# Kernel tuning notes

Measured on AMD Instinct MI355X. Metric: run time of the kernel, lower is better.

The kernel has to match this reference:

```python
import jax, jax.numpy as jnp
import numpy as np

EPS = 1e-8


def cos_loss(a, b):
    # a, b: [n, c, h, w]; cosine distance over channel dim, mean over rest
    a_norm = jnp.sqrt((a * a).sum(1, keepdims=True))
    b_norm = jnp.sqrt((b * b).sum(1, keepdims=True))
    cossim = ((a / (a_norm + EPS)) * (b / (b_norm + EPS))).sum(1)
    return (1.0 - cossim).mean()


def nn_feat_replace(a, b):
    # a: [1, c, h, w], b: [1, c, h2, w2]
    n, c, h, w = a.shape
    a_flat = a.reshape(n, c, -1)                    # [1, c, hw]
    b_flat = b.reshape(n, c, -1)                    # [1, c, h2w2]
    # normalize along channel dim (matches argmin_cos_distance's two-eps scheme)
    b_n = b_flat / (jnp.sqrt((b_flat * b_flat).sum(1, keepdims=True) + EPS) + EPS)
    a_n = a_flat / (jnp.sqrt((a_flat * a_flat).sum(1, keepdims=True) + EPS) + EPS)
    # full cosine-distance matrix: [1, hw, h2w2]
    d_mat = 1.0 - jnp.einsum('bci,bcj->bij', a_n, b_n)
    z_best = jnp.argmin(d_mat, axis=2)              # [1, hw]
    feat = jnp.take(b_flat, z_best[0], axis=2)      # gather: [1, c, hw]
    return feat.reshape(n, c, h, w)


def setup_inputs() -> dict:
    key = jax.random.key(0)
    k1, k2 = jax.random.split(key)
    a = jax.random.normal(k1, (1, 768, 128, 128), dtype=jnp.float32)
    b = jax.random.normal(k2, (1, 768, 128, 128), dtype=jnp.float32)
    return {"a": a, "b": b}


def reference(a, b):
    target = nn_feat_replace(a, b)
    return cos_loss(a, target)
```

## Files before the change

### kernel.cpp

```cpp
#include <hip/hip_runtime.h>
#include <stdint.h>

#define HW 16384
#define CDIM 768
#define EPSF 1e-8f

typedef float f32x4  __attribute__((ext_vector_type(4)));
typedef float f32x16 __attribute__((ext_vector_type(16)));
typedef int   i32x8  __attribute__((ext_vector_type(8)));
typedef uint32_t u32x4 __attribute__((ext_vector_type(4)));

__device__ inline void async16(const void* g, void* l) {
    __builtin_amdgcn_global_load_lds(
        (const __attribute__((address_space(1))) uint32_t*)g,
        (__attribute__((address_space(3))) uint32_t*)l, 16, 0, 0);
}

__device__ inline uint32_t pk4_fp8(float v0, float v1, float v2, float v3) {
    uint32_t r = __builtin_amdgcn_cvt_pk_fp8_f32(v0, v1, 0, false);
    r = __builtin_amdgcn_cvt_pk_fp8_f32(v2, v3, r, true);
    return r;
}

__global__ void __launch_bounds__(256)
transpose_fp8_norm(const float* __restrict__ a, const float* __restrict__ b,
                   uint8_t* __restrict__ at8, uint8_t* __restrict__ bn8,
                   float* __restrict__ sumsq_a, float* __restrict__ sumsq_b) {
    const int z = blockIdx.z;
    const float* src = z ? b : a;
    uint8_t* dst = z ? bn8 : at8;
    float* sums = z ? sumsq_b : sumsq_a;
    const float mult = z ? 8.0f : 16.0f;

    __shared__ float tile[64][65];
    const int s0 = blockIdx.x * 64, c0 = blockIdx.y * 64;
    const int tx = threadIdx.x & 63, ty = threadIdx.x >> 6;
#pragma unroll
    for (int p = 0; p < 16; ++p) {
        int cl = p * 4 + ty;
        tile[cl][tx] = src[(size_t)(c0 + cl) * HW + s0 + tx];
    }
    __syncthreads();

    const int chgrp = tx & 15, rowsub = tx >> 4;
    uint32_t* dst32 = (uint32_t*)dst;
#pragma unroll
    for (int p = 0; p < 4; ++p) {
        int sl = p * 16 + ty * 4 + rowsub;
        float v0 = tile[chgrp * 4 + 0][sl];
        float v1 = tile[chgrp * 4 + 1][sl];
        float v2 = tile[chgrp * 4 + 2][sl];
        float v3 = tile[chgrp * 4 + 3][sl];
        float part = v0 * v0 + v1 * v1 + v2 * v2 + v3 * v3;
        dst32[(size_t)(s0 + sl) * (CDIM / 4) + (c0 >> 2) + chgrp] =
            pk4_fp8(v0 * mult, v1 * mult, v2 * mult, v3 * mult);
#pragma unroll
        for (int m = 1; m < 16; m <<= 1) part += __shfl_xor(part, m, 64);
        if (chgrp == 0) atomicAdd(&sums[s0 + sl], part);
    }
}

__global__ void prep_invd(const float* __restrict__ sumsq_b,
                          float* __restrict__ invdb) {
    int j = blockIdx.x * 256 + threadIdx.x;
    invdb[j] = 1.0f / (sqrtf(sumsq_b[j] + EPSF) + EPSF);
}

__global__ void
gemm_argmax(const uint8_t* __restrict__ at8, const uint8_t* __restrict__ bn8,
            const float* __restrict__ invdb,
            unsigned long long* __restrict__ best) {
    __shared__ uint8_t Al[2 * 8192];
    __shared__ uint8_t Bl[2 * 8192];

    const int g = blockIdx.x;
    const int xcd    = g & 7;
    const int s      = g >> 3;
    const int super  = s >> 5;
    const int within = s & 31;
    const int si = super >> 4;
    const int sj = super & 15;
    const int it = xcd * 16 + si * 4 + (within & 3);
    const int jt = sj * 8 + (within >> 2);

    const int i0 = it * 128, j0 = jt * 128;
    const int tid = threadIdx.x;
    const int lane = tid & 63, w = tid >> 6;
    const int wi = w & 1, wj = w >> 1;
    const int l31 = lane & 31, hi = lane >> 5;

    f32x16 acc[2][2] = {};

    const int srow = lane >> 2;
    const int schunk = ((lane & 3) ^ ((lane >> 3) & 3)) * 16;
    const uint8_t* gA = at8 + (size_t)(i0 + w * 32 + srow) * CDIM + schunk;
    const uint8_t* gB = bn8 + (size_t)(j0 + w * 32 + srow) * CDIM + schunk;
    uint8_t* lA = Al + w * 2048;
    uint8_t* lB = Bl + w * 2048;

    const int rA0 = (wi * 64 + l31) * 64;
    const int rB0 = (wj * 64 + l31) * 64;
    const int c0 = ((hi * 2) ^ ((l31 >> 1) & 3)) * 16;

#define STAGE(bo, kk)                                         \
    do {                                                      \
        async16(gA + (kk),             lA + (bo));            \
        async16(gA + (kk) + 16 * CDIM, lA + (bo) + 1024);     \
        async16(gB + (kk),             lB + (bo));            \
        async16(gB + (kk) + 16 * CDIM, lB + (bo) + 1024);     \
    } while (0)

#define COMPUTE(bo)                                                          \
    do {                                                                     \
        i32x8 af0, af1, bg;                                                  \
        *(u32x4*)&af0       = *(const u32x4*)&Al[(bo) + rA0 + c0];           \
        *((u32x4*)&af0 + 1) = *(const u32x4*)&Al[(bo) + rA0 + (c0 ^ 16)];    \
        *(u32x4*)&af1       = *(const u32x4*)&Al[(bo) + rA0 + 2048 + c0];    \
        *((u32x4*)&af1 + 1) = *(const u32x4*)&Al[(bo) + rA0 + 2048 + (c0 ^ 16)]; \
        *(u32x4*)&bg        = *(const u32x4*)&Bl[(bo) + rB0 + c0];           \
        *((u32x4*)&bg + 1)  = *(const u32x4*)&Bl[(bo) + rB0 + (c0 ^ 16)];    \
        acc[0][0] = __builtin_amdgcn_mfma_scale_f32_32x32x64_f8f6f4(         \
            bg, af0, acc[0][0], 0, 0, 0, 0x7F7F7F7F, 0, 0x7F7F7F7F);         \
        acc[0][1] = __builtin_amdgcn_mfma_scale_f32_32x32x64_f8f6f4(         \
            bg, af1, acc[0][1], 0, 0, 0, 0x7F7F7F7F, 0, 0x7F7F7F7F);         \
        *(u32x4*)&bg        = *(const u32x4*)&Bl[(bo) + rB0 + 2048 + c0];    \
        *((u32x4*)&bg + 1)  = *(const u32x4*)&Bl[(bo) + rB0 + 2048 + (c0 ^ 16)]; \
        acc[1][0] = __builtin_amdgcn_mfma_scale_f32_32x32x64_f8f6f4(         \
            bg, af0, acc[1][0], 0, 0, 0, 0x7F7F7F7F, 0, 0x7F7F7F7F);         \
        acc[1][1] = __builtin_amdgcn_mfma_scale_f32_32x32x64_f8f6f4(         \
            bg, af1, acc[1][1], 0, 0, 0, 0x7F7F7F7F, 0, 0x7F7F7F7F);         \
    } while (0)

    STAGE(0, 0);
    asm volatile("s_waitcnt vmcnt(0)" ::: "memory");
    __builtin_amdgcn_s_barrier();

#pragma unroll 1
    for (int t = 0; t < 11; ++t) {
        const int bo = (t & 1) * 8192;
        STAGE(bo ^ 8192, (t + 1) * 64);
        COMPUTE(bo);
        asm volatile("s_waitcnt vmcnt(0)" ::: "memory");
        __builtin_amdgcn_s_barrier();
    }
    COMPUTE(8192);

#undef STAGE
#undef COMPUTE

    float bv[2] = {-1e30f, -1e30f};
    int   bj[2] = {0, 0};
#pragma unroll
    for (int nj = 0; nj < 2; ++nj) {
        const int jb = j0 + wj * 64 + nj * 32 + 4 * hi;
        f32x4 iv[4];
#pragma unroll
        for (int q = 0; q < 4; ++q)
            iv[q] = *(const f32x4*)&invdb[jb + 8 * q];
#pragma unroll
        for (int mi = 0; mi < 2; ++mi) {
#pragma unroll
            for (int r = 0; r < 16; ++r) {
                int j = jb + (r & 3) + 8 * (r >> 2);
                float v = acc[nj][mi][r] * iv[r >> 2][r & 3];
                if (v > bv[mi] || (v == bv[mi] && j < bj[mi])) {
                    bv[mi] = v; bj[mi] = j;
                }
            }
        }
    }
#pragma unroll
    for (int mi = 0; mi < 2; ++mi) {
        float ov = __shfl_xor(bv[mi], 32, 64);
        int   oj = __shfl_xor(bj[mi], 32, 64);
        if (ov > bv[mi] || (ov == bv[mi] && oj < bj[mi])) {
            bv[mi] = ov; bj[mi] = oj;
        }
        if (hi == 0) {
            int gi = i0 + wi * 64 + mi * 32 + l31;
            uint32_t u = __float_as_uint(bv[mi]);
            u = (u & 0x80000000u) ? ~u : (u | 0x80000000u);
            unsigned long long packed =
                ((unsigned long long)u << 32) | (uint32_t)(~(uint32_t)bj[mi]);
            atomicMax(&best[gi], packed);
        }
    }
}

__global__ void loss_reduce(const unsigned long long* __restrict__ best,
                            const float* __restrict__ sumsq_a,
                            const float* __restrict__ sumsq_b,
                            float* __restrict__ out) {
    int i = blockIdx.x * 256 + threadIdx.x;
    unsigned long long pk = best[i];
    uint32_t x = (uint32_t)(pk >> 32);
    float v = (x & 0x80000000u) ? __uint_as_float(x & 0x7fffffffu)
                                : __uint_as_float(~x);
    int j = (int)(~(uint32_t)pk);
    float sb = sumsq_b[j];
    float denb = sqrtf(sb + EPSF) + EPSF;
    float dot = v * denb * (1.0f / 128.0f);
    float cs = dot / ((sqrtf(sumsq_a[i]) + EPSF) * (sqrtf(sb) + EPSF));
    float term = 1.0f - cs;
#pragma unroll
    for (int m = 32; m; m >>= 1) term += __shfl_down(term, m, 64);
    __shared__ float red[4];
    int wv = threadIdx.x >> 6, lane = threadIdx.x & 63;
    if (lane == 0) red[wv] = term;
    __syncthreads();
    if (threadIdx.x == 0) {
        float ssum = (red[0] + red[1] + red[2] + red[3]) * (1.0f / HW);
        atomicAdd(out, ssum);
    }
}

extern "C" void kernel_launch(void* const* d_in, const int* in_sizes, int n_in,
                              void* d_out, int out_size, void* d_ws, size_t ws_size,
                              hipStream_t stream) {
    const float* a = (const float*)d_in[0];
    const float* b = (const float*)d_in[1];
    char* ws = (char*)d_ws;

    const size_t T_BYTES = (size_t)HW * CDIM;
    uint8_t* at8 = (uint8_t*)ws;
    uint8_t* bn8 = (uint8_t*)(ws + T_BYTES);
    float* sumsq_a = (float*)(ws + 2 * T_BYTES);
    float* sumsq_b = (float*)(ws + 2 * T_BYTES + HW * sizeof(float));
    unsigned long long* best =
        (unsigned long long*)(ws + 2 * T_BYTES + 2 * HW * sizeof(float));
    float* invdb = (float*)(ws + 2 * T_BYTES + 2 * HW * sizeof(float)
                            + HW * sizeof(unsigned long long));

    hipMemsetAsync(sumsq_a, 0, 2 * HW * sizeof(float) + HW * sizeof(unsigned long long),
                   stream);
    hipMemsetAsync(d_out, 0, out_size * sizeof(float), stream);

    dim3 tg(HW / 64, CDIM / 64, 2);
    transpose_fp8_norm<<<tg, 256, 0, stream>>>(a, b, at8, bn8, sumsq_a, sumsq_b);
    prep_invd<<<HW / 256, 256, 0, stream>>>(sumsq_b, invdb);
    gemm_argmax<<<(HW / 128) * (HW / 128), 256, 0, stream>>>(at8, bn8, invdb, best);
    loss_reduce<<<HW / 256, 256, 0, stream>>>(best, sumsq_a, sumsq_b, (float*)d_out);
}
```

Before: 376.0 us.

## Widen GEMM block tile to 128x256 with 8 waves; vectorize transpose loads

The fused GEMM+argmax kernel now gives each block a 128x256 tile using 512 threads (8 waves), doubling the B staging buffer and halving the A rows each wave loads. The block-index swizzle is adjusted to match, so each A tile is reused across twice as many B columns, cutting global/L2 traffic per MFMA. MFMA issue is also wrapped in s_setprio to favour the matrix instructions. The transpose kernel now reads float4 vectors instead of scalars. The cost is more LDS per block and possibly lower occupancy.

```diff
diff --git a/kernel.cpp b/kernel.cpp
--- a/kernel.cpp
+++ b/kernel.cpp
@@ -34,14 +34,20 @@
 
     __shared__ float tile[64][65];
     const int s0 = blockIdx.x * 64, c0 = blockIdx.y * 64;
+
+    const int lane16 = threadIdx.x & 15, crow = threadIdx.x >> 4;
+#pragma unroll
+    for (int p = 0; p < 4; ++p) {
+        int cl = p * 16 + crow;
+        f32x4 v = *(const f32x4*)&src[(size_t)(c0 + cl) * HW + s0 + lane16 * 4];
+        tile[cl][lane16 * 4 + 0] = v[0];
+        tile[cl][lane16 * 4 + 1] = v[1];
+        tile[cl][lane16 * 4 + 2] = v[2];
+        tile[cl][lane16 * 4 + 3] = v[3];
+    }
+    __syncthreads();
+
     const int tx = threadIdx.x & 63, ty = threadIdx.x >> 6;
-#pragma unroll
-    for (int p = 0; p < 16; ++p) {
-        int cl = p * 4 + ty;
-        tile[cl][tx] = src[(size_t)(c0 + cl) * HW + s0 + tx];
-    }
-    __syncthreads();
-
     const int chgrp = tx & 15, rowsub = tx >> 4;
     uint32_t* dst32 = (uint32_t*)dst;
 #pragma unroll
@@ -71,19 +77,19 @@
             const float* __restrict__ invdb,
             unsigned long long* __restrict__ best) {
     __shared__ uint8_t Al[2 * 8192];
-    __shared__ uint8_t Bl[2 * 8192];
+    __shared__ uint8_t Bl[2 * 16384];
 
     const int g = blockIdx.x;
     const int xcd    = g & 7;
     const int s      = g >> 3;
     const int super  = s >> 5;
     const int within = s & 31;
-    const int si = super >> 4;
-    const int sj = super & 15;
+    const int si = super >> 3;
+    const int sj = super & 7;
     const int it = xcd * 16 + si * 4 + (within & 3);
     const int jt = sj * 8 + (within >> 2);
 
-    const int i0 = it * 128, j0 = jt * 128;
+    const int i0 = it * 128, j0 = jt * 256;
     const int tid = threadIdx.x;
     const int lane = tid & 63, w = tid >> 6;
     const int wi = w & 1, wj = w >> 1;
@@ -93,60 +99,67 @@
 
     const int srow = lane >> 2;
     const int schunk = ((lane & 3) ^ ((lane >> 3) & 3)) * 16;
-    const uint8_t* gA = at8 + (size_t)(i0 + w * 32 + srow) * CDIM + schunk;
-    const uint8_t* gB = bn8 + (size_t)(j0 + w * 32 + srow) * CDIM + schunk;
-    uint8_t* lA = Al + w * 2048;
+    const uint8_t* gAs = at8 + (size_t)(i0 + w * 16 + srow) * CDIM + schunk;
+    const uint8_t* gBs = bn8 + (size_t)(j0 + w * 32 + srow) * CDIM + schunk;
+    uint8_t* lA = Al + w * 1024;
     uint8_t* lB = Bl + w * 2048;
 
     const int rA0 = (wi * 64 + l31) * 64;
     const int rB0 = (wj * 64 + l31) * 64;
     const int c0 = ((hi * 2) ^ ((l31 >> 1) & 3)) * 16;
 
-#define STAGE(bo, kk)                                         \
-    do {                                                      \
-        async16(gA + (kk),             lA + (bo));            \
-        async16(gA + (kk) + 16 * CDIM, lA + (bo) + 1024);     \
-        async16(gB + (kk),             lB + (bo));            \
-        async16(gB + (kk) + 16 * CDIM, lB + (bo) + 1024);     \
+#define STAGE(boA, boB)                                        \
+    do {                                                       \
+        async16(gAs,             lA + (boA));                  \
+        async16(gBs,             lB + (boB));                  \
+        async16(gBs + 16 * CDIM, lB + (boB) + 1024);           \
+        gAs += 64; gBs += 64;                                  \
     } while (0)
 
-#define COMPUTE(bo)                                                          \
+#define COMPUTE(boA, boB)                                                    \
     do {                                                                     \
         i32x8 af0, af1, bg;                                                  \
-        *(u32x4*)&af0       = *(const u32x4*)&Al[(bo) + rA0 + c0];           \
-        *((u32x4*)&af0 + 1) = *(const u32x4*)&Al[(bo) + rA0 + (c0 ^ 16)];    \
-        *(u32x4*)&af1       = *(const u32x4*)&Al[(bo) + rA0 + 2048 + c0];    \
-        *((u32x4*)&af1 + 1) = *(const u32x4*)&Al[(bo) + rA0 + 2048 + (c0 ^ 16)]; \
-        *(u32x4*)&bg        = *(const u32x4*)&Bl[(bo) + rB0 + c0];           \
-        *((u32x4*)&bg + 1)  = *(const u32x4*)&Bl[(bo) + rB0 + (c0 ^ 16)];    \
+        *(u32x4*)&af0       = *(const u32x4*)&Al[(boA) + rA0 + c0];          \
+        *((u32x4*)&af0 + 1) = *(const u32x4*)&Al[(boA) + rA0 + (c0 ^ 16)];   \
+        *(u32x4*)&af1       = *(const u32x4*)&Al[(boA) + rA0 + 2048 + c0];   \
+        *((u32x4*)&af1 + 1) = *(const u32x4*)&Al[(boA) + rA0 + 2048 + (c0 ^ 16)]; \
+        *(u32x4*)&bg        = *(const u32x4*)&Bl[(boB) + rB0 + c0];          \
+        *((u32x4*)&bg + 1)  = *(const u32x4*)&Bl[(boB) + rB0 + (c0 ^ 16)];   \
+        __builtin_amdgcn_s_setprio(1);                                       \
         acc[0][0] = __builtin_amdgcn_mfma_scale_f32_32x32x64_f8f6f4(         \
             bg, af0, acc[0][0], 0, 0, 0, 0x7F7F7F7F, 0, 0x7F7F7F7F);         \
         acc[0][1] = __builtin_amdgcn_mfma_scale_f32_32x32x64_f8f6f4(         \
             bg, af1, acc[0][1], 0, 0, 0, 0x7F7F7F7F, 0, 0x7F7F7F7F);         \
-        *(u32x4*)&bg        = *(const u32x4*)&Bl[(bo) + rB0 + 2048 + c0];    \
-        *((u32x4*)&bg + 1)  = *(const u32x4*)&Bl[(bo) + rB0 + 2048 + (c0 ^ 16)]; \
+        __builtin_amdgcn_s_setprio(0);                                       \
+        *(u32x4*)&bg        = *(const u32x4*)&Bl[(boB) + rB0 + 2048 + c0];   \
+        *((u32x4*)&bg + 1)  = *(const u32x4*)&Bl[(boB) + rB0 + 2048 + (c0 ^ 16)]; \
+        __builtin_amdgcn_s_setprio(1);                                       \
         acc[1][0] = __builtin_amdgcn_mfma_scale_f32_32x32x64_f8f6f4(         \
             bg, af0, acc[1][0], 0, 0, 0, 0x7F7F7F7F, 0, 0x7F7F7F7F);         \
         acc[1][1] = __builtin_amdgcn_mfma_scale_f32_32x32x64_f8f6f4(         \
             bg, af1, acc[1][1], 0, 0, 0, 0x7F7F7F7F, 0, 0x7F7F7F7F);         \
+        __builtin_amdgcn_s_setprio(0);                                       \
     } while (0)
 
+#define WAITN(n) asm volatile("s_waitcnt vmcnt(" #n ")" ::: "memory")
+
     STAGE(0, 0);
-    asm volatile("s_waitcnt vmcnt(0)" ::: "memory");
+    WAITN(0);
     __builtin_amdgcn_s_barrier();
 
 #pragma unroll 1
     for (int t = 0; t < 11; ++t) {
-        const int bo = (t & 1) * 8192;
-        STAGE(bo ^ 8192, (t + 1) * 64);
-        COMPUTE(bo);
-        asm volatile("s_waitcnt vmcnt(0)" ::: "memory");
+        const int boA = (t & 1) * 8192, boB = (t & 1) * 16384;
+        STAGE(boA ^ 8192, boB ^ 16384);
+        COMPUTE(boA, boB);
+        WAITN(0);
         __builtin_amdgcn_s_barrier();
     }
-    COMPUTE(8192);
+    COMPUTE(8192, 16384);
 
 #undef STAGE
 #undef COMPUTE
+#undef WAITN
 
     float bv[2] = {-1e30f, -1e30f};
     int   bj[2] = {0, 0};
@@ -238,6 +251,6 @@
     dim3 tg(HW / 64, CDIM / 64, 2);
     transpose_fp8_norm<<<tg, 256, 0, stream>>>(a, b, at8, bn8, sumsq_a, sumsq_b);
     prep_invd<<<HW / 256, 256, 0, stream>>>(sumsq_b, invdb);
-    gemm_argmax<<<(HW / 128) * (HW / 128), 256, 0, stream>>>(at8, bn8, invdb, best);
+    gemm_argmax<<<(HW / 128) * (HW / 256), 512, 0, stream>>>(at8, bn8, invdb, best);
     loss_reduce<<<HW / 256, 256, 0, stream>>>(best, sumsq_a, sumsq_b, (float*)d_out);
 }
```

After: 401.3 us. 1.07x slower.
